# Kernel optimization log

Measured on AMD Instinct MI355X. Metric: run time of the kernel, lower is better.

## Reference

```python
import jax, jax.numpy as jnp
import numpy as np

N = 150_000      # nodes
E = 4_800_000    # edges (avg degree 32)
F_IN = 3
H = 16           # hidden_dim (module default)
DEPTH = 2        # -> DEPTH-1 = 1 mid layer


def setup_inputs() -> dict:
    key = jax.random.key(0)
    ks = jax.random.split(key, 6)
    x = jax.random.normal(ks[0], (N, F_IN), dtype=jnp.float32)
    edge_index = jax.random.randint(ks[1], (2, E), 0, N, dtype=jnp.int64)
    W_in = jax.random.normal(ks[2], (F_IN, H), dtype=jnp.float32) / np.sqrt(F_IN)
    b_in = jnp.zeros((H,), jnp.float32)
    W_mid = jax.random.normal(ks[3], (DEPTH - 1, H, H), dtype=jnp.float32) / np.sqrt(H)
    b_mid = jnp.zeros((DEPTH - 1, H), jnp.float32)
    W_out = jax.random.normal(ks[4], (H, 1), dtype=jnp.float32) / np.sqrt(H)
    b_out = jnp.zeros((1,), jnp.float32)
    return dict(x=x, edge_index=edge_index, W_in=W_in, b_in=b_in,
                W_mid=W_mid, b_mid=b_mid, W_out=W_out, b_out=b_out)


def _gcn(x, src, dst, norm, W, b):
    # GCNConv: X' = D^{-1/2}(A+I)D^{-1/2} X W + b  (self loops already in src/dst)
    h = x @ W                                   # [N, out]
    msg = h[src] * norm[:, None]                # gather + scale, [E+N, out]
    agg = jax.ops.segment_sum(msg, dst, num_segments=N)  # scatter-add
    return agg + b


def reference(x, edge_index, W_in, b_in, W_mid, b_mid, W_out, b_out):
    loops = jnp.arange(N, dtype=edge_index.dtype)
    src = jnp.concatenate([edge_index[0], loops])
    dst = jnp.concatenate([edge_index[1], loops])
    deg = jax.ops.segment_sum(jnp.ones_like(dst, x.dtype), dst, num_segments=N)
    dinv = jax.lax.rsqrt(jnp.where(deg > 0, deg, 1.0))  # deg >= 1 due to self loops
    norm = dinv[src] * dinv[dst]                # symmetric normalization per edge

    h = jax.nn.relu(_gcn(x, src, dst, norm, W_in, b_in))
    for i in range(DEPTH - 1):                  # dropout p=0.0 -> identity
        h = jax.nn.relu(_gcn(h, src, dst, norm, W_mid[i], b_mid[i]))
    out = _gcn(h, src, dst, norm, W_out, b_out)
    return jax.nn.sigmoid(out)                  # [N, 1]
```

## Files before the change

kernel.cpp:

```cpp
#include <hip/hip_runtime.h>
#include <math.h>

#define NN 150000
#define NE 4800000
#define HD 16
#define NBUCK 586
#define BSH 8
#define NBLK 256
#define CHUNK 18750
#define NSCAN 150016
#define SCANB 147

__device__ __forceinline__ float bf2f(unsigned short u) {
    return __uint_as_float(((unsigned int)u) << 16);
}
__device__ __forceinline__ unsigned short f2bf(float f) {
    unsigned int x = __float_as_uint(f);
    return (unsigned short)((x + 0x7FFFu + ((x >> 16) & 1u)) >> 16);
}


__global__ __launch_bounds__(512) void k_part_count(const int* __restrict__ dst,
                                                    int* __restrict__ C) {
    __shared__ int h[NBUCK];
    for (int i = threadIdx.x; i < NBUCK; i += 512) h[i] = 0;
    __syncthreads();
    int base = blockIdx.x * CHUNK;
    for (int i = threadIdx.x; i < CHUNK; i += 512)
        atomicAdd(&h[dst[base + i] >> BSH], 1);
    __syncthreads();
    for (int i = threadIdx.x; i < NBUCK; i += 512) C[i * NBLK + blockIdx.x] = h[i];
}

__global__ void k_scanA(int* __restrict__ C, int* __restrict__ psum) {
    __shared__ int s[1024];
    int t = threadIdx.x;
    int i = blockIdx.x * 1024 + t;
    int v = (i < NSCAN) ? C[i] : 0;
    s[t] = v;
    __syncthreads();
    for (int off = 1; off < 1024; off <<= 1) {
        int x = (t >= off) ? s[t - off] : 0;
        __syncthreads();
        s[t] += x;
        __syncthreads();
    }
    if (i < NSCAN) C[i] = s[t] - v;
    if (t == 1023) psum[blockIdx.x] = s[1023];
}

__global__ void k_scanB(int* __restrict__ psum) {
    __shared__ int s[512];
    int t = threadIdx.x;
    int v = (t < SCANB) ? psum[t] : 0;
    s[t] = v;
    __syncthreads();
    for (int off = 1; off < 512; off <<= 1) {
        int x = (t >= off) ? s[t - off] : 0;
        __syncthreads();
        s[t] += x;
        __syncthreads();
    }
    if (t < SCANB) psum[t] = s[t] - v;
}

__global__ void k_scanC(int* __restrict__ C, const int* __restrict__ psum,
                        int* __restrict__ bstart) {
    int i = blockIdx.x * 1024 + threadIdx.x;
    if (i >= NSCAN) return;
    int v = C[i] + psum[blockIdx.x];
    C[i] = v;
    if ((i & (NBLK - 1)) == 0) bstart[i >> BSH] = v;
    if (i == 0) bstart[NBUCK] = NE;
}

__global__ __launch_bounds__(512) void k_part_scatter(const int* __restrict__ src,
                                                      const int* __restrict__ dst,
                                                      const int* __restrict__ C,
                                                      int* __restrict__ packed) {
    __shared__ int cur[NBUCK];
    int bid = blockIdx.x;
    int m = ((bid & 7) << 5) | (bid >> 3);
    for (int i = threadIdx.x; i < NBUCK; i += 512) cur[i] = C[i * NBLK + m];
    __syncthreads();
    int base = m * CHUNK;
    for (int i = threadIdx.x; i < CHUNK; i += 512) {
        int s = src[base + i], d = dst[base + i];
        int pos = atomicAdd(&cur[d >> BSH], 1);
        packed[pos] = (s << BSH) | (d & 255);
    }
}

__global__ __launch_bounds__(256) void k_bucket_sort(const int* __restrict__ packed,
                                                     const int* __restrict__ bstart,
                                                     int* __restrict__ row_start,
                                                     float* __restrict__ dinv,
                                                     int* __restrict__ ssrc) {
    __shared__ int hist[256];
    __shared__ int fill[256];
    int b = blockIdx.x;
    int t = threadIdx.x;
    int v0 = b << BSH;
    int nv = min(256, NN - v0);
    int e0 = bstart[b], e1 = bstart[b + 1];
    hist[t] = 0;
    __syncthreads();
    for (int e = e0 + t; e < e1; e += 256)
        atomicAdd(&hist[packed[e] & 255], 1);
    __syncthreads();
    int cv = hist[t];
    __syncthreads();
    for (int off = 1; off < 256; off <<= 1) {
        int x = (t >= off) ? hist[t - off] : 0;
        __syncthreads();
        hist[t] += x;
        __syncthreads();
    }
    int excl = hist[t] - cv;
    if (t < nv) {
        row_start[v0 + t] = e0 + excl;
        fill[t] = e0 + excl;
        dinv[v0 + t] = rsqrtf((float)cv + 1.0f);
    }
    __syncthreads();
    for (int e = e0 + t; e < e1; e += 256) {
        int p = packed[e];
        int pos = atomicAdd(&fill[p & 255], 1);
        ssrc[pos] = p >> BSH;
    }
    if (b == 0 && t == 0) row_start[NN] = NE;
}

__global__ __launch_bounds__(256) void k_transform_in(const float* __restrict__ x,
                                                      const float* __restrict__ W,
                                                      const float* __restrict__ dinv,
                                                      unsigned short* __restrict__ t) {
    int gid = blockIdx.x * blockDim.x + threadIdx.x;
    if (gid >= NN * HD) return;
    int v = gid >> 4, j = gid & 15;
    float s = x[v * 3 + 0] * W[j] + x[v * 3 + 1] * W[HD + j] + x[v * 3 + 2] * W[2 * HD + j];
    t[gid] = f2bf(s * dinv[v]);
}

__global__ __launch_bounds__(512) void k_gather_mid(const int* __restrict__ row_start,
                                                    const int* __restrict__ ssrc,
                                                    const unsigned short* __restrict__ t,
                                                    const float* __restrict__ dinv,
                                                    const float* __restrict__ b,
                                                    const float* __restrict__ W,
                                                    unsigned short* __restrict__ tnext) {
    __shared__ float sW[HD * HD];
    __shared__ float sh[16 * HD];
    int tid = threadIdx.x;
    if (tid < HD * HD) sW[tid] = W[tid];
    int node = tid >> 5;
    int lane = tid & 31;
    int sub  = lane >> 3;
    int fl   = lane & 7;
    int v = blockIdx.x * 16 + node;
    int e0 = row_start[v], e1 = row_start[v + 1];
    float sx = 0.0f, sy = 0.0f;
    int e = e0 + sub;
    for (; e + 4 < e1; e += 8) {
        int sA = ssrc[e], sB = ssrc[e + 4];
        unsigned int wA = *(const unsigned int*)(t + (size_t)sA * HD + 2 * fl);
        unsigned int wB = *(const unsigned int*)(t + (size_t)sB * HD + 2 * fl);
        sx += bf2f((unsigned short)wA) + bf2f((unsigned short)wB);
        sy += bf2f((unsigned short)(wA >> 16)) + bf2f((unsigned short)(wB >> 16));
    }
    for (; e < e1; e += 4) {
        unsigned int w = *(const unsigned int*)(t + (size_t)ssrc[e] * HD + 2 * fl);
        sx += bf2f((unsigned short)w);
        sy += bf2f((unsigned short)(w >> 16));
    }
    if (sub == 0) {
        unsigned int w = *(const unsigned int*)(t + (size_t)v * HD + 2 * fl);
        sx += bf2f((unsigned short)w);
        sy += bf2f((unsigned short)(w >> 16));
    }
    sx += __shfl_xor(sx, 8);  sx += __shfl_xor(sx, 16);
    sy += __shfl_xor(sy, 8);  sy += __shfl_xor(sy, 16);
    if (sub == 0) {
        float di = dinv[v];
        sh[node * HD + 2 * fl]     = fmaxf(sx * di + b[2 * fl], 0.0f);
        sh[node * HD + 2 * fl + 1] = fmaxf(sy * di + b[2 * fl + 1], 0.0f);
    }
    __syncthreads();
    if (tid < 256) {
        int n = tid >> 4, jj = tid & 15;
        int vv = blockIdx.x * 16 + n;
        float o = 0.0f;
#pragma unroll
        for (int k = 0; k < HD; ++k) o += sh[n * HD + k] * sW[k * HD + jj];
        tnext[(size_t)vv * HD + jj] = f2bf(o * dinv[vv]);
    }
}

__global__ __launch_bounds__(512) void k_gather_out(const int* __restrict__ row_start,
                                                    const int* __restrict__ ssrc,
                                                    const unsigned short* __restrict__ t,
                                                    const float* __restrict__ dinv,
                                                    const float* __restrict__ b,
                                                    const float* __restrict__ Wout,
                                                    float* __restrict__ t3) {
    int tid = threadIdx.x;
    int node = tid >> 5;
    int lane = tid & 31;
    int sub  = lane >> 3;
    int fl   = lane & 7;
    int v = blockIdx.x * 16 + node;
    int e0 = row_start[v], e1 = row_start[v + 1];
    float sx = 0.0f, sy = 0.0f;
    int e = e0 + sub;
    for (; e + 4 < e1; e += 8) {
        int sA = ssrc[e], sB = ssrc[e + 4];
        unsigned int wA = *(const unsigned int*)(t + (size_t)sA * HD + 2 * fl);
        unsigned int wB = *(const unsigned int*)(t + (size_t)sB * HD + 2 * fl);
        sx += bf2f((unsigned short)wA) + bf2f((unsigned short)wB);
        sy += bf2f((unsigned short)(wA >> 16)) + bf2f((unsigned short)(wB >> 16));
    }
    for (; e < e1; e += 4) {
        unsigned int w = *(const unsigned int*)(t + (size_t)ssrc[e] * HD + 2 * fl);
        sx += bf2f((unsigned short)w);
        sy += bf2f((unsigned short)(w >> 16));
    }
    if (sub == 0) {
        unsigned int w = *(const unsigned int*)(t + (size_t)v * HD + 2 * fl);
        sx += bf2f((unsigned short)w);
        sy += bf2f((unsigned short)(w >> 16));
    }
    sx += __shfl_xor(sx, 8);  sx += __shfl_xor(sx, 16);
    sy += __shfl_xor(sy, 8);  sy += __shfl_xor(sy, 16);
    float di = dinv[v];
    float hx = fmaxf(sx * di + b[2 * fl], 0.0f);
    float hy = fmaxf(sy * di + b[2 * fl + 1], 0.0f);
    float d = hx * Wout[2 * fl] + hy * Wout[2 * fl + 1];
    d += __shfl_xor(d, 1);
    d += __shfl_xor(d, 2);
    d += __shfl_xor(d, 4);
    if (lane == 0) t3[v] = d * di;
}

__global__ __launch_bounds__(256) void k_gather_final(const int* __restrict__ row_start,
                                                      const int* __restrict__ ssrc,
                                                      const float* __restrict__ t3,
                                                      const float* __restrict__ dinv,
                                                      const float* __restrict__ b_out,
                                                      float* __restrict__ out) {
    int tid = threadIdx.x;
    int v = blockIdx.x * 16 + (tid >> 4);
    int l = tid & 15;
    int e0 = row_start[v], e1 = row_start[v + 1];
    float sum = 0.0f;
    for (int e = e0 + l; e < e1; e += 16) sum += t3[ssrc[e]];
    sum += __shfl_xor(sum, 1);
    sum += __shfl_xor(sum, 2);
    sum += __shfl_xor(sum, 4);
    sum += __shfl_xor(sum, 8);
    if (l == 0) {
        float z = (sum + t3[v]) * dinv[v] + b_out[0];
        out[v] = 1.0f / (1.0f + expf(-z));
    }
}

extern "C" void kernel_launch(void* const* d_in, const int* in_sizes, int n_in,
                              void* d_out, int out_size, void* d_ws, size_t ws_size,
                              hipStream_t stream) {
    const float* x     = (const float*)d_in[0];
    const int*   ei    = (const int*)d_in[1];
    const float* W_in  = (const float*)d_in[2];
    const float* b_in  = (const float*)d_in[3];
    const float* W_mid = (const float*)d_in[4];
    const float* b_mid = (const float*)d_in[5];
    const float* W_out = (const float*)d_in[6];
    const float* b_out = (const float*)d_in[7];
    float* out = (float*)d_out;

    const int* src = ei;
    const int* dst = ei + NE;

    char* p = (char*)d_ws;
    int*   C         = (int*)p;      p += sizeof(int) * NSCAN;
    int*   psum      = (int*)p;      p += sizeof(int) * 160;
    int*   bstart    = (int*)p;      p += sizeof(int) * (NBUCK + 2);
    int*   row_start = (int*)p;      p += sizeof(int) * (NN + 1);
    float* dinv      = (float*)p;    p += sizeof(float) * NN;
    int*   ssrc      = (int*)p;      p += sizeof(int) * (size_t)NE;
    int*   packed    = (int*)p;      p += sizeof(int) * (size_t)NE;
    unsigned short* tA = (unsigned short*)packed;
    unsigned short* tB = tA + (size_t)NN * HD;
    float* t3          = (float*)(tB + (size_t)NN * HD);

    const int gNH = (NN * HD + 255) / 256;
    const int gV  = NN / 16;

    k_part_count<<<NBLK, 512, 0, stream>>>(dst, C);
    k_scanA<<<SCANB, 1024, 0, stream>>>(C, psum);
    k_scanB<<<1, 512, 0, stream>>>(psum);
    k_scanC<<<SCANB, 1024, 0, stream>>>(C, psum, bstart);
    k_part_scatter<<<NBLK, 512, 0, stream>>>(src, dst, C, packed);
    k_bucket_sort<<<NBUCK, 256, 0, stream>>>(packed, bstart, row_start, dinv, ssrc);

    k_transform_in<<<gNH, 256, 0, stream>>>(x, W_in, dinv, tA);
    k_gather_mid<<<gV, 512, 0, stream>>>(row_start, ssrc, tA, dinv, b_in, W_mid, tB);
    k_gather_out<<<gV, 512, 0, stream>>>(row_start, ssrc, tB, dinv, b_mid, W_out, t3);
    k_gather_final<<<gV, 256, 0, stream>>>(row_start, ssrc, t3, dinv, b_out, out);
}
```

Measured before the change: 331.8 us.

## Split node features into two 8-wide planes and gather each plane separately

Node features are stored as two bf16 planes of 8 features each instead of one interleaved 16-wide row. Each layer's gather now runs as two passes, one per plane. Each pass writes fp32 partial sums, and a separate per-node kernel then applies the bias, ReLU and the dense transform. The aim is to halve the feature table touched per gather pass so it stays resident in cache for random source reads. In exchange, the edge list is read twice per layer and there are extra fp32 sums buffers plus extra kernel launches.

Result: slower. 373.4 us (+12.5%).

```diff
diff --git a/kernel.cpp b/kernel.cpp
--- a/kernel.cpp
+++ b/kernel.cpp
@@ -10,6 +10,7 @@
 #define CHUNK 18750
 #define NSCAN 150016
 #define SCANB 147
+#define PL ((size_t)NN * 8)
 
 __device__ __forceinline__ float bf2f(unsigned short u) {
     return __uint_as_float(((unsigned int)u) << 16);
@@ -134,111 +135,150 @@
 __global__ __launch_bounds__(256) void k_transform_in(const float* __restrict__ x,
                                                       const float* __restrict__ W,
                                                       const float* __restrict__ dinv,
-                                                      unsigned short* __restrict__ t) {
+                                                      unsigned short* __restrict__ tA) {
     int gid = blockIdx.x * blockDim.x + threadIdx.x;
     if (gid >= NN * HD) return;
     int v = gid >> 4, j = gid & 15;
     float s = x[v * 3 + 0] * W[j] + x[v * 3 + 1] * W[HD + j] + x[v * 3 + 2] * W[2 * HD + j];
-    t[gid] = f2bf(s * dinv[v]);
-}
-
-__global__ __launch_bounds__(512) void k_gather_mid(const int* __restrict__ row_start,
-                                                    const int* __restrict__ ssrc,
-                                                    const unsigned short* __restrict__ t,
-                                                    const float* __restrict__ dinv,
-                                                    const float* __restrict__ b,
-                                                    const float* __restrict__ W,
-                                                    unsigned short* __restrict__ tnext) {
-    __shared__ float sW[HD * HD];
-    __shared__ float sh[16 * HD];
+    tA[(size_t)(j >> 3) * PL + (size_t)v * 8 + (j & 7)] = f2bf(s * dinv[v]);
+}
+
+__global__ __launch_bounds__(512) void k_gather_plane(const int* __restrict__ row_start,
+                                                      const int* __restrict__ ssrc,
+                                                      const unsigned short* __restrict__ plane,
+                                                      float* __restrict__ sums) {
     int tid = threadIdx.x;
-    if (tid < HD * HD) sW[tid] = W[tid];
     int node = tid >> 5;
     int lane = tid & 31;
-    int sub  = lane >> 3;
-    int fl   = lane & 7;
+    int sub  = lane >> 2;
+    int fl   = lane & 3;
     int v = blockIdx.x * 16 + node;
     int e0 = row_start[v], e1 = row_start[v + 1];
     float sx = 0.0f, sy = 0.0f;
     int e = e0 + sub;
-    for (; e + 4 < e1; e += 8) {
-        int sA = ssrc[e], sB = ssrc[e + 4];
-        unsigned int wA = *(const unsigned int*)(t + (size_t)sA * HD + 2 * fl);
-        unsigned int wB = *(const unsigned int*)(t + (size_t)sB * HD + 2 * fl);
+    for (; e + 8 < e1; e += 16) {
+        int sA = ssrc[e], sB = ssrc[e + 8];
+        unsigned int wA = *(const unsigned int*)(plane + (size_t)sA * 8 + 2 * fl);
+        unsigned int wB = *(const unsigned int*)(plane + (size_t)sB * 8 + 2 * fl);
         sx += bf2f((unsigned short)wA) + bf2f((unsigned short)wB);
         sy += bf2f((unsigned short)(wA >> 16)) + bf2f((unsigned short)(wB >> 16));
     }
-    for (; e < e1; e += 4) {
-        unsigned int w = *(const unsigned int*)(t + (size_t)ssrc[e] * HD + 2 * fl);
+    for (; e < e1; e += 8) {
+        unsigned int w = *(const unsigned int*)(plane + (size_t)ssrc[e] * 8 + 2 * fl);
         sx += bf2f((unsigned short)w);
         sy += bf2f((unsigned short)(w >> 16));
     }
+    sx += __shfl_xor(sx, 4);  sx += __shfl_xor(sx, 8);  sx += __shfl_xor(sx, 16);
+    sy += __shfl_xor(sy, 4);  sy += __shfl_xor(sy, 8);  sy += __shfl_xor(sy, 16);
     if (sub == 0) {
-        unsigned int w = *(const unsigned int*)(t + (size_t)v * HD + 2 * fl);
-        sx += bf2f((unsigned short)w);
-        sy += bf2f((unsigned short)(w >> 16));
-    }
-    sx += __shfl_xor(sx, 8);  sx += __shfl_xor(sx, 16);
-    sy += __shfl_xor(sy, 8);  sy += __shfl_xor(sy, 16);
-    if (sub == 0) {
-        float di = dinv[v];
-        sh[node * HD + 2 * fl]     = fmaxf(sx * di + b[2 * fl], 0.0f);
-        sh[node * HD + 2 * fl + 1] = fmaxf(sy * di + b[2 * fl + 1], 0.0f);
-    }
-    __syncthreads();
-    if (tid < 256) {
-        int n = tid >> 4, jj = tid & 15;
-        int vv = blockIdx.x * 16 + n;
-        float o = 0.0f;
-#pragma unroll
-        for (int k = 0; k < HD; ++k) o += sh[n * HD + k] * sW[k * HD + jj];
-        tnext[(size_t)vv * HD + jj] = f2bf(o * dinv[vv]);
-    }
-}
-
-__global__ __launch_bounds__(512) void k_gather_out(const int* __restrict__ row_start,
-                                                    const int* __restrict__ ssrc,
-                                                    const unsigned short* __restrict__ t,
+        sums[(size_t)v * 8 + 2 * fl]     = sx;
+        sums[(size_t)v * 8 + 2 * fl + 1] = sy;
+    }
+}
+
+__global__ __launch_bounds__(256) void k_mlp_mid(const float* __restrict__ sums0,
+                                                 const float* __restrict__ sums1,
+                                                 const unsigned short* __restrict__ tA,
+                                                 const float* __restrict__ dinv,
+                                                 const float* __restrict__ b,
+                                                 const float* __restrict__ W,
+                                                 unsigned short* __restrict__ tB) {
+    __shared__ float sW[256];
+    __shared__ float sb[16];
+    int tid = threadIdx.x;
+    sW[tid] = W[tid];
+    if (tid < 16) sb[tid] = b[tid];
+    __syncthreads();
+    int v = blockIdx.x * 256 + tid;
+    if (v >= NN) return;
+    float di = dinv[v];
+    float h[16];
+    const float4* s0 = (const float4*)(sums0 + (size_t)v * 8);
+    const float4* s1 = (const float4*)(sums1 + (size_t)v * 8);
+    uint4 a0 = *(const uint4*)(tA + (size_t)v * 8);
+    uint4 a1 = *(const uint4*)(tA + PL + (size_t)v * 8);
+#pragma unroll
+    for (int q = 0; q < 2; ++q) {
+        float4 s = s0[q];
+        unsigned int w0 = (&a0.x)[2 * q], w1 = (&a0.x)[2 * q + 1];
+        h[4 * q + 0] = fmaxf((s.x + bf2f((unsigned short)w0))         * di + sb[4 * q + 0], 0.0f);
+        h[4 * q + 1] = fmaxf((s.y + bf2f((unsigned short)(w0 >> 16))) * di + sb[4 * q + 1], 0.0f);
+        h[4 * q + 2] = fmaxf((s.z + bf2f((unsigned short)w1))         * di + sb[4 * q + 2], 0.0f);
+        h[4 * q + 3] = fmaxf((s.w + bf2f((unsigned short)(w1 >> 16))) * di + sb[4 * q + 3], 0.0f);
+    }
+#pragma unroll
+    for (int q = 0; q < 2; ++q) {
+        float4 s = s1[q];
+        unsigned int w0 = (&a1.x)[2 * q], w1 = (&a1.x)[2 * q + 1];
+        h[8 + 4 * q + 0] = fmaxf((s.x + bf2f((unsigned short)w0))         * di + sb[8 + 4 * q + 0], 0.0f);
+        h[8 + 4 * q + 1] = fmaxf((s.y + bf2f((unsigned short)(w0 >> 16))) * di + sb[8 + 4 * q + 1], 0.0f);
+        h[8 + 4 * q + 2] = fmaxf((s.z + bf2f((unsigned short)w1))         * di + sb[8 + 4 * q + 2], 0.0f);
+        h[8 + 4 * q + 3] = fmaxf((s.w + bf2f((unsigned short)(w1 >> 16))) * di + sb[8 + 4 * q + 3], 0.0f);
+    }
+    uint4 o0, o1;
+#pragma unroll
+    for (int p = 0; p < 4; ++p) {
+        float oa = 0.0f, ob = 0.0f;
+#pragma unroll
+        for (int k = 0; k < 16; ++k) {
+            oa += h[k] * sW[k * 16 + 2 * p];
+            ob += h[k] * sW[k * 16 + 2 * p + 1];
+        }
+        (&o0.x)[p] = (unsigned int)f2bf(oa * di) | ((unsigned int)f2bf(ob * di) << 16);
+    }
+#pragma unroll
+    for (int p = 0; p < 4; ++p) {
+        float oa = 0.0f, ob = 0.0f;
+#pragma unroll
+        for (int k = 0; k < 16; ++k) {
+            oa += h[k] * sW[k * 16 + 8 + 2 * p];
+            ob += h[k] * sW[k * 16 + 8 + 2 * p + 1];
+        }
+        (&o1.x)[p] = (unsigned int)f2bf(oa * di) | ((unsigned int)f2bf(ob * di) << 16);
+    }
+    *(uint4*)(tB + (size_t)v * 8)      = o0;
+    *(uint4*)(tB + PL + (size_t)v * 8) = o1;
+}
+
+__global__ __launch_bounds__(256) void k_out_finish(const float* __restrict__ sums0,
+                                                    const float* __restrict__ sums1,
+                                                    const unsigned short* __restrict__ tB,
                                                     const float* __restrict__ dinv,
                                                     const float* __restrict__ b,
                                                     const float* __restrict__ Wout,
                                                     float* __restrict__ t3) {
+    __shared__ float sW[16];
+    __shared__ float sb[16];
     int tid = threadIdx.x;
-    int node = tid >> 5;
-    int lane = tid & 31;
-    int sub  = lane >> 3;
-    int fl   = lane & 7;
-    int v = blockIdx.x * 16 + node;
-    int e0 = row_start[v], e1 = row_start[v + 1];
-    float sx = 0.0f, sy = 0.0f;
-    int e = e0 + sub;
-    for (; e + 4 < e1; e += 8) {
-        int sA = ssrc[e], sB = ssrc[e + 4];
-        unsigned int wA = *(const unsigned int*)(t + (size_t)sA * HD + 2 * fl);
-        unsigned int wB = *(const unsigned int*)(t + (size_t)sB * HD + 2 * fl);
-        sx += bf2f((unsigned short)wA) + bf2f((unsigned short)wB);
-        sy += bf2f((unsigned short)(wA >> 16)) + bf2f((unsigned short)(wB >> 16));
-    }
-    for (; e < e1; e += 4) {
-        unsigned int w = *(const unsigned int*)(t + (size_t)ssrc[e] * HD + 2 * fl);
-        sx += bf2f((unsigned short)w);
-        sy += bf2f((unsigned short)(w >> 16));
-    }
-    if (sub == 0) {
-        unsigned int w = *(const unsigned int*)(t + (size_t)v * HD + 2 * fl);
-        sx += bf2f((unsigned short)w);
-        sy += bf2f((unsigned short)(w >> 16));
-    }
-    sx += __shfl_xor(sx, 8);  sx += __shfl_xor(sx, 16);
-    sy += __shfl_xor(sy, 8);  sy += __shfl_xor(sy, 16);
+    if (tid < 16) { sW[tid] = Wout[tid]; sb[tid] = b[tid]; }
+    __syncthreads();
+    int v = blockIdx.x * 256 + tid;
+    if (v >= NN) return;
     float di = dinv[v];
-    float hx = fmaxf(sx * di + b[2 * fl], 0.0f);
-    float hy = fmaxf(sy * di + b[2 * fl + 1], 0.0f);
-    float d = hx * Wout[2 * fl] + hy * Wout[2 * fl + 1];
-    d += __shfl_xor(d, 1);
-    d += __shfl_xor(d, 2);
-    d += __shfl_xor(d, 4);
-    if (lane == 0) t3[v] = d * di;
+    const float4* s0 = (const float4*)(sums0 + (size_t)v * 8);
+    const float4* s1 = (const float4*)(sums1 + (size_t)v * 8);
+    uint4 a0 = *(const uint4*)(tB + (size_t)v * 8);
+    uint4 a1 = *(const uint4*)(tB + PL + (size_t)v * 8);
+    float acc = 0.0f;
+#pragma unroll
+    for (int q = 0; q < 2; ++q) {
+        float4 s = s0[q];
+        unsigned int w0 = (&a0.x)[2 * q], w1 = (&a0.x)[2 * q + 1];
+        acc += fmaxf((s.x + bf2f((unsigned short)w0))         * di + sb[4 * q + 0], 0.0f) * sW[4 * q + 0];
+        acc += fmaxf((s.y + bf2f((unsigned short)(w0 >> 16))) * di + sb[4 * q + 1], 0.0f) * sW[4 * q + 1];
+        acc += fmaxf((s.z + bf2f((unsigned short)w1))         * di + sb[4 * q + 2], 0.0f) * sW[4 * q + 2];
+        acc += fmaxf((s.w + bf2f((unsigned short)(w1 >> 16))) * di + sb[4 * q + 3], 0.0f) * sW[4 * q + 3];
+    }
+#pragma unroll
+    for (int q = 0; q < 2; ++q) {
+        float4 s = s1[q];
+        unsigned int w0 = (&a1.x)[2 * q], w1 = (&a1.x)[2 * q + 1];
+        acc += fmaxf((s.x + bf2f((unsigned short)w0))         * di + sb[8 + 4 * q + 0], 0.0f) * sW[8 + 4 * q + 0];
+        acc += fmaxf((s.y + bf2f((unsigned short)(w0 >> 16))) * di + sb[8 + 4 * q + 1], 0.0f) * sW[8 + 4 * q + 1];
+        acc += fmaxf((s.z + bf2f((unsigned short)w1))         * di + sb[8 + 4 * q + 2], 0.0f) * sW[8 + 4 * q + 2];
+        acc += fmaxf((s.w + bf2f((unsigned short)(w1 >> 16))) * di + sb[8 + 4 * q + 3], 0.0f) * sW[8 + 4 * q + 3];
+    }
+    t3[v] = acc * di;
 }
 
 __global__ __launch_bounds__(256) void k_gather_final(const int* __restrict__ row_start,
@@ -287,12 +327,15 @@
     float* dinv      = (float*)p;    p += sizeof(float) * NN;
     int*   ssrc      = (int*)p;      p += sizeof(int) * (size_t)NE;
     int*   packed    = (int*)p;      p += sizeof(int) * (size_t)NE;
+    float* sums0     = (float*)p;    p += sizeof(float) * PL;
+    float* sums1     = (float*)p;    p += sizeof(float) * PL;
     unsigned short* tA = (unsigned short*)packed;
-    unsigned short* tB = tA + (size_t)NN * HD;
-    float* t3          = (float*)(tB + (size_t)NN * HD);
+    unsigned short* tB = tA + 2 * PL;
+    float* t3          = (float*)(tB + 2 * PL);
 
     const int gNH = (NN * HD + 255) / 256;
     const int gV  = NN / 16;
+    const int gN  = (NN + 255) / 256;
 
     k_part_count<<<NBLK, 512, 0, stream>>>(dst, C);
     k_scanA<<<SCANB, 1024, 0, stream>>>(C, psum);
@@ -302,7 +345,14 @@
     k_bucket_sort<<<NBUCK, 256, 0, stream>>>(packed, bstart, row_start, dinv, ssrc);
 
     k_transform_in<<<gNH, 256, 0, stream>>>(x, W_in, dinv, tA);
-    k_gather_mid<<<gV, 512, 0, stream>>>(row_start, ssrc, tA, dinv, b_in, W_mid, tB);
-    k_gather_out<<<gV, 512, 0, stream>>>(row_start, ssrc, tB, dinv, b_mid, W_out, t3);
+
+    k_gather_plane<<<gV, 512, 0, stream>>>(row_start, ssrc, tA,      sums0);
+    k_gather_plane<<<gV, 512, 0, stream>>>(row_start, ssrc, tA + PL, sums1);
+    k_mlp_mid<<<gN, 256, 0, stream>>>(sums0, sums1, tA, dinv, b_in, W_mid, tB);
+
+    k_gather_plane<<<gV, 512, 0, stream>>>(row_start, ssrc, tB,      sums0);
+    k_gather_plane<<<gV, 512, 0, stream>>>(row_start, ssrc, tB + PL, sums1);
+    k_out_finish<<<gN, 256, 0, stream>>>(sums0, sums1, tB, dinv, b_mid, W_out, t3);
+
     k_gather_final<<<gV, 256, 0, stream>>>(row_start, ssrc, t3, dinv, b_out, out);
 }
```

## Stage partition scatter through LDS for coalesced writes; add nontemporal streaming loads

Applied to the files above, without the earlier changes.

The partition scatter kernel now handles its chunk in two halves. Each half is counted, locally bucket-sorted into a shared-memory staging array, and then copied out to global memory in contiguous per-bucket runs, replacing the random per-element global writes. Streaming reads of dst, src, packed and ssrc across several kernels now use nontemporal loads so they do not evict the reused feature table from cache. The cost is a second pass over dst, extra shared memory (about 44KB per block, which lowers occupancy) and more barriers.

Measured after the change: 420.7 us. 26.8% more time.

```diff
diff --git a/kernel.cpp b/kernel.cpp
--- a/kernel.cpp
+++ b/kernel.cpp
@@ -8,8 +8,11 @@
 #define BSH 8
 #define NBLK 256
 #define CHUNK 18750
+#define HCH 9375
 #define NSCAN 150016
 #define SCANB 147
+
+#define NTL(x) __builtin_nontemporal_load(&(x))
 
 __device__ __forceinline__ float bf2f(unsigned short u) {
     return __uint_as_float(((unsigned int)u) << 16);
@@ -27,7 +30,7 @@
     __syncthreads();
     int base = blockIdx.x * CHUNK;
     for (int i = threadIdx.x; i < CHUNK; i += 512)
-        atomicAdd(&h[dst[base + i] >> BSH], 1);
+        atomicAdd(&h[NTL(dst[base + i]) >> BSH], 1);
     __syncthreads();
     for (int i = threadIdx.x; i < NBUCK; i += 512) C[i * NBLK + blockIdx.x] = h[i];
 }
@@ -78,16 +81,54 @@
                                                       const int* __restrict__ dst,
                                                       const int* __restrict__ C,
                                                       int* __restrict__ packed) {
-    __shared__ int cur[NBUCK];
+    __shared__ int gcur[NBUCK];
+    __shared__ int lcnt[NBUCK];
+    __shared__ int lofs[NBUCK];
+    __shared__ int stage[HCH];
+    int tid = threadIdx.x;
     int bid = blockIdx.x;
     int m = ((bid & 7) << 5) | (bid >> 3);
-    for (int i = threadIdx.x; i < NBUCK; i += 512) cur[i] = C[i * NBLK + m];
-    __syncthreads();
-    int base = m * CHUNK;
-    for (int i = threadIdx.x; i < CHUNK; i += 512) {
-        int s = src[base + i], d = dst[base + i];
-        int pos = atomicAdd(&cur[d >> BSH], 1);
-        packed[pos] = (s << BSH) | (d & 255);
+    for (int i = tid; i < NBUCK; i += 512) gcur[i] = C[i * NBLK + m];
+    for (int ph = 0; ph < 2; ++ph) {
+        int base = m * CHUNK + ph * HCH;
+        for (int i = tid; i < NBUCK; i += 512) lcnt[i] = 0;
+        __syncthreads();
+        for (int i = tid; i < HCH; i += 512)
+            atomicAdd(&lcnt[NTL(dst[base + i]) >> BSH], 1);
+        __syncthreads();
+        if (tid < 64) {
+            int run = 0;
+            for (int b0 = 0; b0 < NBUCK; b0 += 64) {
+                int idx = b0 + tid;
+                int c = (idx < NBUCK) ? lcnt[idx] : 0;
+                int inc = c;
+#pragma unroll
+                for (int off = 1; off < 64; off <<= 1) {
+                    int y = __shfl_up(inc, off);
+                    if (tid >= off) inc += y;
+                }
+                if (idx < NBUCK) lofs[idx] = run + inc - c;
+                run += __shfl(inc, 63);
+            }
+        }
+        __syncthreads();
+        for (int i = tid; i < HCH; i += 512) {
+            int s = NTL(src[base + i]);
+            int d = NTL(dst[base + i]);
+            int b = d >> BSH;
+            int pos = atomicAdd(&lofs[b], 1);
+            stage[pos] = (s << BSH) | (d & 255);
+        }
+        __syncthreads();
+        int wv = tid >> 6, ln = tid & 63;
+        for (int b = wv; b < NBUCK; b += 8) {
+            int c = lcnt[b];
+            int ls = lofs[b] - c;
+            int gs = gcur[b];
+            for (int k = ln; k < c; k += 64) packed[gs + k] = stage[ls + k];
+        }
+        __syncthreads();
+        for (int i = tid; i < NBUCK; i += 512) gcur[i] += lcnt[i];
     }
 }
 
@@ -106,7 +147,7 @@
     hist[t] = 0;
     __syncthreads();
     for (int e = e0 + t; e < e1; e += 256)
-        atomicAdd(&hist[packed[e] & 255], 1);
+        atomicAdd(&hist[NTL(packed[e]) & 255], 1);
     __syncthreads();
     int cv = hist[t];
     __syncthreads();
@@ -124,7 +165,7 @@
     }
     __syncthreads();
     for (int e = e0 + t; e < e1; e += 256) {
-        int p = packed[e];
+        int p = NTL(packed[e]);
         int pos = atomicAdd(&fill[p & 255], 1);
         ssrc[pos] = p >> BSH;
     }
@@ -162,14 +203,14 @@
     float sx = 0.0f, sy = 0.0f;
     int e = e0 + sub;
     for (; e + 4 < e1; e += 8) {
-        int sA = ssrc[e], sB = ssrc[e + 4];
+        int sA = NTL(ssrc[e]), sB = NTL(ssrc[e + 4]);
         unsigned int wA = *(const unsigned int*)(t + (size_t)sA * HD + 2 * fl);
         unsigned int wB = *(const unsigned int*)(t + (size_t)sB * HD + 2 * fl);
         sx += bf2f((unsigned short)wA) + bf2f((unsigned short)wB);
         sy += bf2f((unsigned short)(wA >> 16)) + bf2f((unsigned short)(wB >> 16));
     }
     for (; e < e1; e += 4) {
-        unsigned int w = *(const unsigned int*)(t + (size_t)ssrc[e] * HD + 2 * fl);
+        unsigned int w = *(const unsigned int*)(t + (size_t)NTL(ssrc[e]) * HD + 2 * fl);
         sx += bf2f((unsigned short)w);
         sy += bf2f((unsigned short)(w >> 16));
     }
@@ -213,14 +254,14 @@
     float sx = 0.0f, sy = 0.0f;
     int e = e0 + sub;
     for (; e + 4 < e1; e += 8) {
-        int sA = ssrc[e], sB = ssrc[e + 4];
+        int sA = NTL(ssrc[e]), sB = NTL(ssrc[e + 4]);
         unsigned int wA = *(const unsigned int*)(t + (size_t)sA * HD + 2 * fl);
         unsigned int wB = *(const unsigned int*)(t + (size_t)sB * HD + 2 * fl);
         sx += bf2f((unsigned short)wA) + bf2f((unsigned short)wB);
         sy += bf2f((unsigned short)(wA >> 16)) + bf2f((unsigned short)(wB >> 16));
     }
     for (; e < e1; e += 4) {
-        unsigned int w = *(const unsigned int*)(t + (size_t)ssrc[e] * HD + 2 * fl);
+        unsigned int w = *(const unsigned int*)(t + (size_t)NTL(ssrc[e]) * HD + 2 * fl);
         sx += bf2f((unsigned short)w);
         sy += bf2f((unsigned short)(w >> 16));
     }
@@ -252,7 +293,7 @@
     int l = tid & 15;
     int e0 = row_start[v], e1 = row_start[v + 1];
     float sum = 0.0f;
-    for (int e = e0 + l; e < e1; e += 16) sum += t3[ssrc[e]];
+    for (int e = e0 + l; e < e1; e += 16) sum += t3[NTL(ssrc[e])];
     sum += __shfl_xor(sum, 1);
     sum += __shfl_xor(sum, 2);
     sum += __shfl_xor(sum, 4);
```
